# Optimization experiments

Measured on AMD Instinct MI355X. Metric: run time of the kernel, lower is better.

The kernel has to match this reference:

```python
import jax, jax.numpy as jnp
import numpy as np

B, N, F = 2, 2048, 256
H = 8
O = F // H  # nhid = 32
L = 3       # stacked GraphAttentionLayers
ALPHA = 0.2
NEG = jnp.float32(-1e15)


def setup_inputs() -> dict:
    key = jax.random.key(0)
    ks = jax.random.split(key, 6)
    x = jax.random.normal(ks[0], (B, N, F), dtype=jnp.float32)
    adj = jax.random.randint(ks[1], (B, N, N), 0, 2, dtype=jnp.int32)
    # per-layer multi-head params: W [L,H,F,O], a [L,H,2O]
    W_heads = jax.random.normal(ks[2], (L, H, F, O), dtype=jnp.float32) * 0.1
    a_heads = jax.random.normal(ks[3], (L, H, 2 * O), dtype=jnp.float32) * 0.1
    # per-layer out_att params (single head, F->F)
    W_out = jax.random.normal(ks[4], (L, F, F), dtype=jnp.float32) * 0.05
    a_out = jax.random.normal(ks[5], (L, 2 * F), dtype=jnp.float32) * 0.05
    return {"x": x, "adj": adj, "W_heads": W_heads, "a_heads": a_heads,
            "W_out": W_out, "a_out": a_out}


def _gat_heads(h, mask, W, a1, a2):
    """h: [B,N,F], mask: [B,N,N] bool, W: [H,F,O], a1/a2: [H,O] -> [B,H,N,O]."""
    Wh = jnp.einsum('bnf,hfo->bhno', h, W)
    s1 = jnp.einsum('bhno,ho->bhn', Wh, a1)   # a[:O] projection
    s2 = jnp.einsum('bhno,ho->bhn', Wh, a2)   # a[O:] projection
    e = s1[:, :, :, None] + s2[:, :, None, :]  # additive score [B,H,N,N]
    e = jnp.where(e > 0, e, ALPHA * e)         # LeakyReLU(alpha)
    e = jnp.where(mask[:, None, :, :], e, NEG)
    att = jax.nn.softmax(e, axis=-1)           # dropout is identity in eval
    hp = jnp.einsum('bhnm,bhmo->bhno', att, Wh)
    return jax.nn.elu(hp)                      # activate_function inside head


def reference(x, adj, W_heads, a_heads, W_out, a_out):
    mask = adj > 0
    h = x
    for l in range(L):
        a1 = a_heads[l, :, :O]
        a2 = a_heads[l, :, O:]
        hh = _gat_heads(h, mask, W_heads[l], a1, a2)      # [B,H,N,O]
        h = jnp.transpose(hh, (0, 2, 1, 3)).reshape(B, N, F)  # concat heads
        ao1 = a_out[l, :F][None]
        ao2 = a_out[l, F:][None]
        ho = _gat_heads(h, mask, W_out[l][None], ao1, ao2)[:, 0]  # [B,N,F]
        h = jax.nn.elu(ho)  # extra F.elu in GraphAttentionLayer (elu twice)
    return h
```

## Files before the change

kernel.cpp:

```cpp
#include <hip/hip_runtime.h>
#include <math.h>

#if __has_builtin(__builtin_amdgcn_exp2f)
#define EXP2(x) __builtin_amdgcn_exp2f(x)
#else
#define EXP2(x) exp2f(x)
#endif

#define ALPHA_LRELU 0.2f
#define LOG2E 1.4426950408889634f
#define ESHIFT 6.0f
#define BIGM 1024.0f

constexpr int Bc = 2, Nn = 2048, Ff = 256, Hh = 8, Oo = 32;

typedef _Float16 f16;
typedef f16 f16x8 __attribute__((ext_vector_type(8)));
typedef f16 f16x4 __attribute__((ext_vector_type(4)));
typedef float f32x4 __attribute__((ext_vector_type(4)));
typedef unsigned long long u64;
typedef unsigned u32;

__global__ __launch_bounds__(256) void prep_kernel(
    const int* __restrict__ adj, const float* __restrict__ x,
    const float* __restrict__ W_heads, const float* __restrict__ W_out,
    u32* __restrict__ maskT, f16* __restrict__ Af, f16* __restrict__ WTF,
    float* __restrict__ sbuf) {
    const int B = blockIdx.x;
    const int t = threadIdx.x;
    int g = B * 256 + t;
    if (g < 221184) sbuf[g] = 0.f;

    if (B < 768) {
        for (int idx = g; idx < Bc * Nn * Nn; idx += 768 * 256) {
            u64 bl = __ballot(adj[idx] != 0);
            int lane = t & 63;
            int i = (idx >> 11) & 2047;
            int b = idx >> 22;
            int c32 = ((idx & 2047) & ~63) >> 5;
            if (lane == 0)
                maskT[((size_t)b * 64 + c32) * 2048 + i] = (u32)bl;
            else if (lane == 1)
                maskT[((size_t)b * 64 + c32 + 1) * 2048 + i] = (u32)(bl >> 32);
        }
    } else if (B < 896) {
        int w = t >> 6, lane = t & 63;
        int am = lane & 15, aq = lane >> 4;
#pragma unroll
        for (int it = 0; it < 4; ++it) {
            int slot = (B - 768) * 4 + w + it * 512;
            int mt = slot >> 3, c = slot & 7;
            const float* ap = x + ((size_t)mt * 16 + am) * Ff + c * 32 + aq * 8;
            f32x4 v0 = *(const f32x4*)ap;
            f32x4 v1 = *(const f32x4*)(ap + 4);
            f16x8 o;
#pragma unroll
            for (int i = 0; i < 4; ++i) { o[i] = (f16)v0[i]; o[4 + i] = (f16)v1[i]; }
            *(f16x8*)&Af[(size_t)slot * 512 + lane * 8] = o;
        }
    } else {
#pragma unroll
        for (int it = 0; it < 3; ++it) {
            int unit = (B - 896) * 3 + it;
            int y = unit >> 6, bx = unit & 63;
            int ll = y >> 1, st = y & 1;
            int col = bx * 4 + (t >> 6);
            int k0 = (t & 63) * 4;
            const float* src;
            int stride;
            if (st == 0) {
                src = W_heads + (((size_t)ll * Hh + (col >> 5)) * Ff) * Oo + (col & 31);
                stride = Oo;
            } else {
                src = W_out + (size_t)ll * Ff * Ff + col;
                stride = Ff;
            }
            f16x4 v;
#pragma unroll
            for (int i = 0; i < 4; ++i) v[i] = (f16)src[(size_t)(k0 + i) * stride];
            int cg = col >> 4, am = col & 15;
            int c = k0 >> 5, aq = (k0 >> 3) & 3, i0 = k0 & 7;
            *(f16x4*)&WTF[(((size_t)y * 16 + cg) * 8 + c) * 512 +
                          (aq * 16 + am) * 8 + i0] = v;
        }
    }
}

__global__ __launch_bounds__(256) void gemm_wave(
    const f16* __restrict__ Af, const f16* __restrict__ WTF,
    const float* __restrict__ pa, f16* __restrict__ WhFrag,
    float* __restrict__ s1, float* __restrict__ s2,
    int G, int Ofull, int oshift) {
    int t = threadIdx.x;
    int w = t >> 6, lane = t & 63;
    int am = lane & 15, aq = lane >> 4;
    int mt = blockIdx.x * 4 + w;
    int colb = blockIdx.y * 16;

    const f16* ap = Af + (size_t)(mt * 8) * 512 + lane * 8;
    const f16* bp = WTF + (size_t)((colb >> 4) * 8) * 512 + lane * 8;

    f16x8 av[8], bv[8];
#pragma unroll
    for (int c = 0; c < 8; ++c) {
        av[c] = *(const f16x8*)(ap + c * 512);
        bv[c] = *(const f16x8*)(bp + c * 512);
    }
    f32x4 acc = {0.f, 0.f, 0.f, 0.f};
#pragma unroll
    for (int c = 0; c < 8; ++c)
        acc = __builtin_amdgcn_mfma_f32_16x16x32_f16(av[c], bv[c], acc, 0, 0, 0);

    int m0 = mt * 16;
    int b = m0 >> 11;
    int nn0 = (m0 & 2047) + aq * 4;
    int cO = (m0 & 2047) >> 5;
    int aq_p = ((mt & 1) << 1) | (aq >> 1);
    int i0p = (aq & 1) << 2;
    int g = colb >> oshift;
    size_t bg = (size_t)b * G + g;
    int cg = (colb & (Ofull - 1)) >> 4;

    f16x4 c4;
#pragma unroll
    for (int e = 0; e < 4; ++e) c4[e] = (f16)acc[e];
    *(f16x4*)&WhFrag[(((bg * (Ofull >> 4) + cg) * 64 + cO) * 512) +
                     (aq_p * 16 + am) * 8 + i0p] = c4;

    int o0 = (colb & (Ofull - 1)) + am;
    const float* a1p = pa + 2 * (size_t)g * Ofull;
    float a10 = a1p[o0];
    float a20 = a1p[Ofull + o0];
#pragma unroll
    for (int e = 0; e < 4; ++e) {
        float p1 = acc[e] * a10;
        float p2 = acc[e] * a20;
#pragma unroll
        for (int s = 1; s < 16; s <<= 1) {
            p1 += __shfl_xor(p1, s);
            p2 += __shfl_xor(p2, s);
        }
        if (am == 0) {
            size_t sidx = bg * Nn + nn0 + e;
            atomicAdd(&s1[sidx], p1);
            atomicAdd(&s2[sidx], p2);
        }
    }
}

template <int CGW, bool OUT, bool FINAL>
__global__ __launch_bounds__(256) void attn_kernel(
    const f16* __restrict__ WhFrag, const float* __restrict__ s1,
    const float* __restrict__ s2, const u32* __restrict__ maskT,
    float* __restrict__ dst, f16* __restrict__ AfOut) {
    constexpr float C0 = -ESHIFT * LOG2E - BIGM;
    constexpr int NCG = OUT ? 16 : 2;
    constexpr int TSTR = 72;
    __shared__ float Ls[4][2][64];
    __shared__ float As[4][64][2 * CGW * 4];
    __shared__ f16 T[2][16 * TSTR];

    int t = threadIdx.x;
    int w = t >> 6, lane = t & 63;
    int am = lane & 15, aq = lane >> 4;
    int i0 = blockIdx.x * 32;
    int bz = blockIdx.z;
    int b = OUT ? bz : (bz >> 3);
    int cg0 = OUT ? blockIdx.y * CGW : 0;
    int dstcol = OUT ? cg0 * 16 : (bz & 7) * Oo;

    const f16* bp[CGW];
#pragma unroll
    for (int i = 0; i < CGW; ++i)
        bp[i] = WhFrag + ((size_t)bz * NCG + cg0 + i) * 64 * 512 + lane * 8;
    const float* s2p = s2 + (size_t)bz * Nn + aq * 8;
    float s1v0 = s1[(size_t)bz * Nn + i0 + am];
    float s1v1 = s1[(size_t)bz * Nn + i0 + 16 + am];
    const u32* mtp0 = maskT + (size_t)b * 64 * 2048 + i0 + am;
    const u32* mtp1 = mtp0 + 16;

    f32x4 acc[2][CGW] = {};
    float lacc0 = 0.f, lacc1 = 0.f;

    int cbeg = w * 16, cend = cbeg + 16;

    f16x8 xb[CGW], yb[CGW];
    f32x4 xv0, xv1, yv0, yv1;
    u32 xm0, xm1, ym0, ym1;
    auto ld = [&](int c, f16x8 (&bb)[CGW], f32x4& v0, f32x4& v1,
                  u32& m0, u32& m1) {
#pragma unroll
        for (int i = 0; i < CGW; ++i) bb[i] = *(const f16x8*)(bp[i] + c * 512);
        v0 = *(const f32x4*)(s2p + c * 32);
        v1 = *(const f32x4*)(s2p + c * 32 + 4);
        m0 = mtp0[c * 2048];
        m1 = mtp1[c * 2048];
    };
    auto comp = [&](f16x8 (&bb)[CGW], f32x4 v0, f32x4 v1, u32 m0, u32 m1) {
        u32 bits0 = (m0 >> (aq * 8)) & 0xffu;
        u32 bits1 = (m1 >> (aq * 8)) & 0xffu;
        f16x8 af0, af1;
#pragma unroll
        for (int k = 0; k < 8; ++k) {
            float sv = (k < 4 ? v0[k] : v1[k - 4]);
            float x0 = s1v0 + sv;
            float x1 = s1v1 + sv;
            float lr0 = fmaxf(x0, ALPHA_LRELU * x0);
            float lr1 = fmaxf(x1, ALPHA_LRELU * x1);
            float bf0 = (float)((bits0 >> k) & 1u);
            float bf1 = (float)((bits1 >> k) & 1u);
            float p0 = EXP2(fmaf(bf0, BIGM, fmaf(lr0, LOG2E, C0)));
            float p1 = EXP2(fmaf(bf1, BIGM, fmaf(lr1, LOG2E, C0)));
            lacc0 += p0;
            lacc1 += p1;
            af0[k] = (f16)p0;
            af1[k] = (f16)p1;
        }
#pragma unroll
        for (int i = 0; i < CGW; ++i) {
            acc[0][i] = __builtin_amdgcn_mfma_f32_16x16x32_f16(af0, bb[i], acc[0][i], 0, 0, 0);
            acc[1][i] = __builtin_amdgcn_mfma_f32_16x16x32_f16(af1, bb[i], acc[1][i], 0, 0, 0);
        }
    };

    ld(cbeg, xb, xv0, xv1, xm0, xm1);
    ld(cbeg + 1, yb, yv0, yv1, ym0, ym1);
    for (int c = cbeg; c < cend; c += 2) {
        comp(xb, xv0, xv1, xm0, xm1);
        ld(c + 2 < cend ? c + 2 : cbeg, xb, xv0, xv1, xm0, xm1);
        comp(yb, yv0, yv1, ym0, ym1);
        ld(c + 3 < cend ? c + 3 : cbeg, yb, yv0, yv1, ym0, ym1);
    }

    lacc0 += __shfl_xor(lacc0, 16);
    lacc0 += __shfl_xor(lacc0, 32);
    lacc1 += __shfl_xor(lacc1, 16);
    lacc1 += __shfl_xor(lacc1, 32);

    Ls[w][0][lane] = lacc0;
    Ls[w][1][lane] = lacc1;
#pragma unroll
    for (int tt = 0; tt < 2; ++tt)
#pragma unroll
        for (int i = 0; i < CGW; ++i)
#pragma unroll
            for (int e = 0; e < 4; ++e)
                As[w][lane][tt * CGW * 4 + i * 4 + e] = acc[tt][i][e];
    __syncthreads();

    if (w < 2) {
        float lt = Ls[0][w][lane] + Ls[1][w][lane] + Ls[2][w][lane] + Ls[3][w][lane];
        f16* Tw = T[w];
#pragma unroll
        for (int i = 0; i < CGW; ++i) {
            f32x4 a;
#pragma unroll
            for (int e = 0; e < 4; ++e)
                a[e] = As[0][lane][w * CGW * 4 + i * 4 + e] +
                       As[1][lane][w * CGW * 4 + i * 4 + e] +
                       As[2][lane][w * CGW * 4 + i * 4 + e] +
                       As[3][lane][w * CGW * 4 + i * 4 + e];
#pragma unroll
            for (int e = 0; e < 4; ++e) {
                int r = aq * 4 + e;
                float li = __shfl(lt, r);
                float v = a[e] / li;
                v = v > 0.f ? v : __expf(v) - 1.f;
                if (OUT) v = v > 0.f ? v : __expf(v) - 1.f;
                if (FINAL) {
                    dst[((size_t)b * Nn + i0 + w * 16 + r) * Ff + dstcol +
                        i * 16 + am] = v;
                } else {
                    Tw[r * TSTR + i * 16 + am] = (f16)v;
                }
            }
        }
        if (!FINAL) {
            int mt = (b * Nn + i0 + w * 16) >> 4;
#pragma unroll
            for (int s = 0; s < CGW / 2; ++s) {
                f16x8 o = *(const f16x8*)&Tw[am * TSTR + s * 32 + aq * 8];
                int c = (dstcol >> 5) + s;
                *(f16x8*)&AfOut[(size_t)(mt * 8 + c) * 512 + lane * 8] = o;
            }
        }
    }
}

extern "C" void kernel_launch(void* const* d_in, const int* in_sizes, int n_in,
                              void* d_out, int out_size, void* d_ws, size_t ws_size,
                              hipStream_t stream) {
    const float* x = (const float*)d_in[0];
    const int* adj = (const int*)d_in[1];
    const float* W_heads = (const float*)d_in[2];
    const float* a_heads = (const float*)d_in[3];
    const float* W_out = (const float*)d_in[4];
    const float* a_out = (const float*)d_in[5];
    float* out = (float*)d_out;

    float* ws = (float*)d_ws;
    const size_t M = (size_t)Bc * Nn * Ff;
    f16* Af_a = (f16*)ws;
    f16* Af_b = (f16*)(ws + M / 2);
    f16* WhFrag = (f16*)(ws + M);
    u32* maskT = (u32*)(ws + 3 * M / 2);
    f16* WTF = (f16*)(ws + 3 * M / 2 + M / 4);
    float* sbuf = ws + 3 * M / 2 + M / 4 + 196608;
    const size_t SH = (size_t)Bc * Hh * Nn;
    const size_t SO = (size_t)Bc * Nn;
    const size_t SL = 2 * SH + 2 * SO;

    prep_kernel<<<1024, 256, 0, stream>>>(adj, x, W_heads, W_out,
                                          maskT, Af_a, WTF, sbuf);

    for (int l = 0; l < 3; ++l) {
        float* s1h = sbuf + l * SL;
        float* s2h = s1h + SH;
        float* s1o = s2h + SH;
        float* s2o = s1o + SO;

        gemm_wave<<<dim3((Bc * Nn) / 64, Ff / 16), 256, 0, stream>>>(
            Af_a, WTF + (size_t)(2 * l) * Ff * Ff,
            a_heads + (size_t)l * Hh * 2 * Oo, WhFrag, s1h, s2h, Hh, Oo, 5);
        attn_kernel<2, false, false><<<dim3(Nn / 32, 1, Bc * Hh), 256, 0, stream>>>(
            WhFrag, s1h, s2h, maskT, nullptr, Af_b);

        gemm_wave<<<dim3((Bc * Nn) / 64, Ff / 16), 256, 0, stream>>>(
            Af_b, WTF + (size_t)(2 * l + 1) * Ff * Ff,
            a_out + (size_t)l * 2 * Ff, WhFrag, s1o, s2o, 1, Ff, 8);
        if (l == 2) {
            attn_kernel<4, true, true><<<dim3(Nn / 32, Ff / 64, Bc), 256, 0, stream>>>(
                WhFrag, s1o, s2o, maskT, out, nullptr);
        } else {
            attn_kernel<4, true, false><<<dim3(Nn / 32, Ff / 64, Bc), 256, 0, stream>>>(
                WhFrag, s1o, s2o, maskT, nullptr, Af_a);
        }
    }
}
```

Before: 268.3 us.

## Widen GEMM column tile and pack two column groups per attention block

Each GEMM wave now computes two 16-column tiles, so one A-fragment load feeds two MFMAs and the grid halves in y. The out-attention kernel now runs 8 waves per block, with two column-chunk groups sharing the same row block. That amortizes the mask and s2 loads and the exp work per block. The cost is more registers per GEMM wave, larger shared memory and block size in attention, and fewer blocks, which lowers parallelism.

```diff
diff --git a/kernel.cpp b/kernel.cpp
--- a/kernel.cpp
+++ b/kernel.cpp
@@ -95,21 +95,25 @@
     int w = t >> 6, lane = t & 63;
     int am = lane & 15, aq = lane >> 4;
     int mt = blockIdx.x * 4 + w;
-    int colb = blockIdx.y * 16;
+    int colb = blockIdx.y * 32;
 
     const f16* ap = Af + (size_t)(mt * 8) * 512 + lane * 8;
-    const f16* bp = WTF + (size_t)((colb >> 4) * 8) * 512 + lane * 8;
-
-    f16x8 av[8], bv[8];
+    const f16* bp0 = WTF + (size_t)((colb >> 4) * 8) * 512 + lane * 8;
+    const f16* bp1 = bp0 + 8 * 512;
+
+    f16x8 av[8], bv0[8], bv1[8];
 #pragma unroll
     for (int c = 0; c < 8; ++c) {
         av[c] = *(const f16x8*)(ap + c * 512);
-        bv[c] = *(const f16x8*)(bp + c * 512);
-    }
-    f32x4 acc = {0.f, 0.f, 0.f, 0.f};
-#pragma unroll
-    for (int c = 0; c < 8; ++c)
-        acc = __builtin_amdgcn_mfma_f32_16x16x32_f16(av[c], bv[c], acc, 0, 0, 0);
+        bv0[c] = *(const f16x8*)(bp0 + c * 512);
+        bv1[c] = *(const f16x8*)(bp1 + c * 512);
+    }
+    f32x4 acc0 = {0.f, 0.f, 0.f, 0.f}, acc1 = acc0;
+#pragma unroll
+    for (int c = 0; c < 8; ++c) {
+        acc0 = __builtin_amdgcn_mfma_f32_16x16x32_f16(av[c], bv0[c], acc0, 0, 0, 0);
+        acc1 = __builtin_amdgcn_mfma_f32_16x16x32_f16(av[c], bv1[c], acc1, 0, 0, 0);
+    }
 
     int m0 = mt * 16;
     int b = m0 >> 11;
@@ -121,20 +125,22 @@
     size_t bg = (size_t)b * G + g;
     int cg = (colb & (Ofull - 1)) >> 4;
 
-    f16x4 c4;
-#pragma unroll
-    for (int e = 0; e < 4; ++e) c4[e] = (f16)acc[e];
+    f16x4 c40, c41;
+#pragma unroll
+    for (int e = 0; e < 4; ++e) { c40[e] = (f16)acc0[e]; c41[e] = (f16)acc1[e]; }
     *(f16x4*)&WhFrag[(((bg * (Ofull >> 4) + cg) * 64 + cO) * 512) +
-                     (aq_p * 16 + am) * 8 + i0p] = c4;
+                     (aq_p * 16 + am) * 8 + i0p] = c40;
+    *(f16x4*)&WhFrag[(((bg * (Ofull >> 4) + cg + 1) * 64 + cO) * 512) +
+                     (aq_p * 16 + am) * 8 + i0p] = c41;
 
     int o0 = (colb & (Ofull - 1)) + am;
     const float* a1p = pa + 2 * (size_t)g * Ofull;
-    float a10 = a1p[o0];
-    float a20 = a1p[Ofull + o0];
+    float a10 = a1p[o0], a11 = a1p[o0 + 16];
+    float a20 = a1p[Ofull + o0], a21 = a1p[Ofull + o0 + 16];
 #pragma unroll
     for (int e = 0; e < 4; ++e) {
-        float p1 = acc[e] * a10;
-        float p2 = acc[e] * a20;
+        float p1 = acc0[e] * a10 + acc1[e] * a11;
+        float p2 = acc0[e] * a20 + acc1[e] * a21;
 #pragma unroll
         for (int s = 1; s < 16; s <<= 1) {
             p1 += __shfl_xor(p1, s);
@@ -148,25 +154,28 @@
     }
 }
 
-template <int CGW, bool OUT, bool FINAL>
-__global__ __launch_bounds__(256) void attn_kernel(
+template <int CGW, int NW, bool OUT, bool FINAL>
+__global__ __launch_bounds__(NW * 64) void attn_kernel(
     const f16* __restrict__ WhFrag, const float* __restrict__ s1,
     const float* __restrict__ s2, const u32* __restrict__ maskT,
     float* __restrict__ dst, f16* __restrict__ AfOut) {
     constexpr float C0 = -ESHIFT * LOG2E - BIGM;
     constexpr int NCG = OUT ? 16 : 2;
-    constexpr int TSTR = 72;
-    __shared__ float Ls[4][2][64];
-    __shared__ float As[4][64][2 * CGW * 4];
+    constexpr int COLS = (NW / 4) * CGW * 16;
+    constexpr int TSTR = COLS + 8;
+    __shared__ float Ls[NW][2][64];
+    __shared__ float As[NW][64][2 * CGW * 4];
     __shared__ f16 T[2][16 * TSTR];
 
     int t = threadIdx.x;
     int w = t >> 6, lane = t & 63;
     int am = lane & 15, aq = lane >> 4;
+    int ch = w >> 2;
+    int js = w & 3;
     int i0 = blockIdx.x * 32;
     int bz = blockIdx.z;
     int b = OUT ? bz : (bz >> 3);
-    int cg0 = OUT ? blockIdx.y * CGW : 0;
+    int cg0 = OUT ? blockIdx.y * ((NW / 4) * CGW) + ch * CGW : 0;
     int dstcol = OUT ? cg0 * 16 : (bz & 7) * Oo;
 
     const f16* bp[CGW];
@@ -182,7 +191,7 @@
     f32x4 acc[2][CGW] = {};
     float lacc0 = 0.f, lacc1 = 0.f;
 
-    int cbeg = w * 16, cend = cbeg + 16;
+    int cbeg = js * 16, cend = cbeg + 16;
 
     f16x8 xb[CGW], yb[CGW];
     f32x4 xv0, xv1, yv0, yv1;
@@ -248,18 +257,20 @@
                 As[w][lane][tt * CGW * 4 + i * 4 + e] = acc[tt][i][e];
     __syncthreads();
 
-    if (w < 2) {
-        float lt = Ls[0][w][lane] + Ls[1][w][lane] + Ls[2][w][lane] + Ls[3][w][lane];
-        f16* Tw = T[w];
+    if ((w & 3) < 2) {
+        int tt = w & 3;
+        float lt = Ls[ch * 4 + 0][tt][lane] + Ls[ch * 4 + 1][tt][lane] +
+                   Ls[ch * 4 + 2][tt][lane] + Ls[ch * 4 + 3][tt][lane];
+        f16* Tw = T[tt];
 #pragma unroll
         for (int i = 0; i < CGW; ++i) {
             f32x4 a;
 #pragma unroll
             for (int e = 0; e < 4; ++e)
-                a[e] = As[0][lane][w * CGW * 4 + i * 4 + e] +
-                       As[1][lane][w * CGW * 4 + i * 4 + e] +
-                       As[2][lane][w * CGW * 4 + i * 4 + e] +
-                       As[3][lane][w * CGW * 4 + i * 4 + e];
+                a[e] = As[ch * 4 + 0][lane][tt * CGW * 4 + i * 4 + e] +
+                       As[ch * 4 + 1][lane][tt * CGW * 4 + i * 4 + e] +
+                       As[ch * 4 + 2][lane][tt * CGW * 4 + i * 4 + e] +
+                       As[ch * 4 + 3][lane][tt * CGW * 4 + i * 4 + e];
 #pragma unroll
             for (int e = 0; e < 4; ++e) {
                 int r = aq * 4 + e;
@@ -268,18 +279,19 @@
                 v = v > 0.f ? v : __expf(v) - 1.f;
                 if (OUT) v = v > 0.f ? v : __expf(v) - 1.f;
                 if (FINAL) {
-                    dst[((size_t)b * Nn + i0 + w * 16 + r) * Ff + dstcol +
+                    dst[((size_t)b * Nn + i0 + tt * 16 + r) * Ff + dstcol +
                         i * 16 + am] = v;
                 } else {
-                    Tw[r * TSTR + i * 16 + am] = (f16)v;
+                    Tw[r * TSTR + ch * CGW * 16 + i * 16 + am] = (f16)v;
                 }
             }
         }
         if (!FINAL) {
-            int mt = (b * Nn + i0 + w * 16) >> 4;
+            int mt = (b * Nn + i0 + tt * 16) >> 4;
 #pragma unroll
             for (int s = 0; s < CGW / 2; ++s) {
-                f16x8 o = *(const f16x8*)&Tw[am * TSTR + s * 32 + aq * 8];
+                f16x8 o = *(const f16x8*)&Tw[am * TSTR + ch * CGW * 16 +
+                                             s * 32 + aq * 8];
                 int c = (dstcol >> 5) + s;
                 *(f16x8*)&AfOut[(size_t)(mt * 8 + c) * 512 + lane * 8] = o;
             }
@@ -319,20 +331,20 @@
         float* s1o = s2h + SH;
         float* s2o = s1o + SO;
 
-        gemm_wave<<<dim3((Bc * Nn) / 64, Ff / 16), 256, 0, stream>>>(
+        gemm_wave<<<dim3((Bc * Nn) / 64, Ff / 32), 256, 0, stream>>>(
             Af_a, WTF + (size_t)(2 * l) * Ff * Ff,
             a_heads + (size_t)l * Hh * 2 * Oo, WhFrag, s1h, s2h, Hh, Oo, 5);
-        attn_kernel<2, false, false><<<dim3(Nn / 32, 1, Bc * Hh), 256, 0, stream>>>(
+        attn_kernel<2, 4, false, false><<<dim3(Nn / 32, 1, Bc * Hh), 256, 0, stream>>>(
             WhFrag, s1h, s2h, maskT, nullptr, Af_b);
 
-        gemm_wave<<<dim3((Bc * Nn) / 64, Ff / 16), 256, 0, stream>>>(
+        gemm_wave<<<dim3((Bc * Nn) / 64, Ff / 32), 256, 0, stream>>>(
             Af_b, WTF + (size_t)(2 * l + 1) * Ff * Ff,
             a_out + (size_t)l * 2 * Ff, WhFrag, s1o, s2o, 1, Ff, 8);
         if (l == 2) {
-            attn_kernel<4, true, true><<<dim3(Nn / 32, Ff / 64, Bc), 256, 0, stream>>>(
+            attn_kernel<4, 8, true, true><<<dim3(Nn / 32, Ff / 128, Bc), 512, 0, stream>>>(
                 WhFrag, s1o, s2o, maskT, out, nullptr);
         } else {
-            attn_kernel<4, true, false><<<dim3(Nn / 32, Ff / 64, Bc), 256, 0, stream>>>(
+            attn_kernel<4, 8, true, false><<<dim3(Nn / 32, Ff / 128, Bc), 512, 0, stream>>>(
                 WhFrag, s1o, s2o, maskT, nullptr, Af_a);
         }
     }
```

Result: no change. 265.3 us, median of 2 (-1.1%).
